# Optimization experiments

Measured on AMD Instinct MI355X. Metric: run time of the kernel, lower is better.

Reference implementation:

```python
import jax, jax.numpy as jnp
import numpy as np

N, E, F_IN, H, MH, C, G = 100000, 3200000, 128, 32, 64, 10, 64

def _seg_sum(data, ids, num):
    return jax.ops.segment_sum(data, ids, num_segments=num)

def gcn_conv(x, row, col, ew, W, b, n):
    # PyG GCNConv: linear first, then self-loops + symmetric edge-weight norm + scatter-add
    h = x @ W  # [N, H]
    loop = jnp.arange(n)
    r = jnp.concatenate([row, loop])
    c = jnp.concatenate([col, loop])
    w = jnp.concatenate([ew, jnp.ones((n,), dtype=ew.dtype)])
    deg = _seg_sum(w, c, n)
    dinv = jnp.where(deg > 0, jax.lax.rsqrt(deg), 0.0)
    norm = dinv[r] * w * dinv[c]  # [E+N]
    out = _seg_sum(norm[:, None] * h[r], c, n)  # scatter to targets
    return out + b

def setup_inputs():
    key = jax.random.key(0)
    ks = jax.random.split(key, 16)
    inp = {
        "x": jax.random.normal(ks[0], (N, F_IN), dtype=jnp.float32),
        "edge_index": jax.random.randint(ks[1], (2, E), 0, N, dtype=jnp.int64),
        "edge_weight": jax.random.uniform(ks[2], (E,), dtype=jnp.float32),
        "batch": jnp.sort(jax.random.randint(ks[3], (N,), 0, G, dtype=jnp.int64)),
    }
    def lin(k, i, o):
        s = 1.0 / np.sqrt(i)
        k1, k2 = jax.random.split(k)
        return (jax.random.uniform(k1, (i, o), minval=-s, maxval=s, dtype=jnp.float32),
                jax.random.uniform(k2, (o,), minval=-s, maxval=s, dtype=jnp.float32))
    inp["W1"], inp["b1"] = lin(ks[4], F_IN, H)
    inp["W2"], inp["b2"] = lin(ks[5], H, H)
    inp["W3"], inp["b3"] = lin(ks[6], H, H)
    inp["Wm0"], inp["bm0"] = lin(ks[7], H, MH)
    inp["Wm1"], inp["bm1"] = lin(ks[8], MH, MH)
    inp["Wout"], inp["bout"] = lin(ks[9], MH, C)
    return inp

def reference(x, edge_index, edge_weight, batch, W1, b1, W2, b2, W3, b3, Wm0, bm0, Wm1, bm1, Wout, bout):
    row, col = edge_index[0], edge_index[1]
    h = jax.nn.relu(gcn_conv(x, row, col, edge_weight, W1, b1, N))
    h = jax.nn.relu(gcn_conv(h, row, col, edge_weight, W2, b2, N))
    h = gcn_conv(h, row, col, edge_weight, W3, b3, N)
    # global mean pool over graphs
    sums = _seg_sum(h, batch, G)
    counts = _seg_sum(jnp.ones((N,), dtype=h.dtype), batch, G)
    g = sums / jnp.maximum(counts, 1.0)[:, None]
    # dropout p=0.5 is identity at inference (training=False)
    g = jax.nn.relu(g @ Wm0 + bm0)
    g = jax.nn.relu(g @ Wm1 + bm1)
    return g @ Wout + bout
```

## Files before the change

kernel.cpp:

```cpp
#include <hip/hip_runtime.h>

#define NN 100000
#define NE 3200000
#define FIN 128
#define HID 32
#define MH  64
#define NC  10
#define NG  64
#define NBKT 782
#define NBLK 512
#define EPB  (NE / NBLK)
#define SCANL (NBKT * NBLK)
#define SRCMASK 0x1FFFF
#define BCAP 5120

typedef float floatx2 __attribute__((ext_vector_type(2)));

__global__ void init_misc(float* __restrict__ sc) {
    int i = blockIdx.x * 256 + threadIdx.x;
    if (i < NG * HID + NG) sc[i] = 0.0f;
}

__global__ __launch_bounds__(1024)
void hist_bkt(const int* __restrict__ ei, int* __restrict__ cnt2) {
    __shared__ int h[NBKT];
    int tid = threadIdx.x, blk = blockIdx.x;
    for (int b = tid; b < NBKT; b += 1024) h[b] = 0;
    __syncthreads();
    int base = blk * EPB;
    for (int i = tid; i < EPB; i += 1024)
        atomicAdd(&h[ei[NE + base + i] >> 7], 1);
    __syncthreads();
    for (int b = tid; b < NBKT; b += 1024) cnt2[b * NBLK + blk] = h[b];
}

__global__ void scan_block(const int* __restrict__ in, int* __restrict__ out,
                           int* __restrict__ bsum, int n) {
    __shared__ int lds[256];
    int tid = threadIdx.x;
    int base = blockIdx.x * 1024 + tid * 4;
    int v0 = 0, v1 = 0, v2 = 0, v3 = 0;
    if (base + 0 < n) v0 = in[base + 0];
    if (base + 1 < n) v1 = in[base + 1];
    if (base + 2 < n) v2 = in[base + 2];
    if (base + 3 < n) v3 = in[base + 3];
    int s = v0 + v1 + v2 + v3;
    lds[tid] = s;
    __syncthreads();
    for (int off = 1; off < 256; off <<= 1) {
        int val = (tid >= off) ? lds[tid - off] : 0;
        __syncthreads();
        lds[tid] += val;
        __syncthreads();
    }
    int excl = lds[tid] - s;
    if (tid == 255) bsum[blockIdx.x] = lds[255];
    if (base + 0 < n) out[base + 0] = excl;
    if (base + 1 < n) out[base + 1] = excl + v0;
    if (base + 2 < n) out[base + 2] = excl + v0 + v1;
    if (base + 3 < n) out[base + 3] = excl + v0 + v1 + v2;
}

__global__ void scan_top(int* __restrict__ bsum, int nb) {
    int lane = threadIdx.x;
    int carry = 0;
    for (int base = 0; base < nb; base += 64) {
        int i = base + lane;
        int orig = (i < nb) ? bsum[i] : 0;
        int v = orig;
#pragma unroll
        for (int off = 1; off < 64; off <<= 1) {
            int t = __shfl_up(v, off, 64);
            if (lane >= off) v += t;
        }
        if (i < nb) bsum[i] = carry + v - orig;
        carry += __shfl(v, 63, 64);
    }
}

__global__ void scan_add(int* __restrict__ data, const int* __restrict__ bsum, int n) {
    int i = blockIdx.x * 256 + threadIdx.x;
    if (i < n) data[i] += bsum[i >> 10];
}

__global__ __launch_bounds__(1024)
void scatter_bkt(const int* __restrict__ ei, const float* __restrict__ ew,
                 const int* __restrict__ cnt2, const int* __restrict__ scanned,
                 int2* __restrict__ tre) {
    __shared__ int2 pay[EPB];
    __shared__ int scur[NBKT];
    __shared__ int hexc[NBKT];
    __shared__ int gbase[NBKT];
    int tid = threadIdx.x, blk = blockIdx.x;
    int myh = 0;
    if (tid < NBKT) {
        myh = cnt2[tid * NBLK + blk];
        gbase[tid] = scanned[tid * NBLK + blk];
        scur[tid] = myh;
    }
    __syncthreads();
    for (int off = 1; off < NBKT; off <<= 1) {
        int v = (tid < NBKT && tid >= off) ? scur[tid - off] : 0;
        __syncthreads();
        if (tid < NBKT) scur[tid] += v;
        __syncthreads();
    }
    if (tid < NBKT) { int ex = scur[tid] - myh; hexc[tid] = ex; scur[tid] = ex; }
    __syncthreads();
    int base = blk * EPB;
    for (int i = tid; i < EPB; i += 1024) {
        int e = base + i;
        int c = ei[NE + e];
        int r = ei[e];
        unsigned int wb = __float_as_uint(ew[e]);
        int b = c >> 7;
        int j = atomicAdd(&scur[b], 1);
        pay[j] = make_int2(r | ((c & 127) << 17) | ((b & 0xFF) << 24),
                           (int)((wb & ~3u) | ((unsigned)b >> 8)));
    }
    __syncthreads();
    for (int j = tid; j < EPB; j += 1024) {
        int2 q = pay[j];
        int b = (int)((((unsigned)q.y & 3u) << 8) | (((unsigned)q.x >> 24) & 0xFFu));
        int pos = gbase[b] + (j - hexc[b]);
        tre[pos] = make_int2(q.x & 0x00FFFFFF, q.y & ~3);
    }
}

__global__ __launch_bounds__(512)
void deg_k(const int2* __restrict__ tre, const int* __restrict__ scanned,
           float* __restrict__ dinv) {
    __shared__ float dw[128];
    int b = blockIdx.x, tid = threadIdx.x;
    int base = scanned[b * NBLK];
    int end = (b == NBKT - 1) ? NE : scanned[(b + 1) * NBLK];
    if (tid < 128) dw[tid] = 0.f;
    __syncthreads();
    for (int i = base + tid; i < end; i += 512) {
        int2 q = tre[i];
        atomicAdd(&dw[(q.x >> 17) & 127], __int_as_float(q.y));
    }
    __syncthreads();
    if (tid < 128) {
        int node = b * 128 + tid;
        if (node < NN) dinv[node] = rsqrtf(1.0f + dw[tid]);
    }
}

__global__ __launch_bounds__(512)
void sort_k(const int2* __restrict__ tre, const int* __restrict__ scanned,
            const float* __restrict__ dinv,
            unsigned int* __restrict__ srn4, int* __restrict__ rowptr) {
    __shared__ int2 ed[BCAP];
    __shared__ int h[128];
    __shared__ int sc[128];
    __shared__ int cur[128];
    int b = blockIdx.x, tid = threadIdx.x;
    int base = scanned[b * NBLK];
    int end = (b == NBKT - 1) ? NE : scanned[(b + 1) * NBLK];
    int n = end - base;
    bool staged = (n <= BCAP);
    if (tid < 128) h[tid] = 0;
    if (staged)
        for (int i = tid; i < n; i += 512) ed[i] = tre[base + i];
    __syncthreads();
    for (int i = tid; i < n; i += 512) {
        int2 q = staged ? ed[i] : tre[base + i];
        atomicAdd(&h[(q.x >> 17) & 127], 1);
    }
    __syncthreads();
    if (tid < 128) sc[tid] = h[tid];
    __syncthreads();
    for (int off = 1; off < 128; off <<= 1) {
        int v = (tid < 128 && tid >= off) ? sc[tid - off] : 0;
        __syncthreads();
        if (tid < 128) sc[tid] += v;
        __syncthreads();
    }
    if (tid < 128) {
        int node = b * 128 + tid;
        if (node < NN) rowptr[node] = base + sc[tid];
        cur[tid] = base + sc[tid] - h[tid];
    }
    __syncthreads();
    for (int i = tid; i < n; i += 512) {
        int2 q = staged ? ed[i] : tre[base + i];
        int key = (q.x >> 17) & 127;
        int pos = atomicAdd(&cur[key], 1);
        unsigned int src = (unsigned)(q.x & SRCMASK);
        float w = __int_as_float(q.y) * dinv[src];
        unsigned int wb = __float_as_uint(w);
        wb += 0x7FFFu + ((wb >> 16) & 1u);
        srn4[pos] = src | (((wb >> 16) & 0x7FFFu) << 17);
    }
}

template <int IN_DIM, bool RELU_IN>
__global__ __launch_bounds__(256)
void linear_k(const float* __restrict__ in, const float* __restrict__ W,
              unsigned int* __restrict__ tmp8) {
    constexpr int J4 = IN_DIM / 4;
    constexpr int XSS = J4 + 1;
    __shared__ float4 xs[64 * XSS];
    __shared__ float4 wp[IN_DIM * 8];
    int tid = threadIdx.x;
    for (int idx = tid; idx < IN_DIM * 8; idx += 256) {
        int j = idx >> 3, kg = idx & 7;
        const float* wr = W + j * 32 + kg * 4;
        wp[idx] = make_float4(wr[0], wr[1], wr[2], wr[3]);
    }
    int rbase = blockIdx.x * 64;
    const float4* in4 = (const float4*)in;
    for (int idx = tid; idx < 64 * J4; idx += 256) {
        int row = idx / J4, j4 = idx % J4;
        int grow = rbase + row;
        float4 v = (grow < NN) ? in4[(size_t)grow * J4 + j4]
                               : make_float4(0.f, 0.f, 0.f, 0.f);
        if (RELU_IN) {
            v.x = fmaxf(v.x, 0.f); v.y = fmaxf(v.y, 0.f);
            v.z = fmaxf(v.z, 0.f); v.w = fmaxf(v.w, 0.f);
        }
        xs[row * XSS + j4] = v;
    }
    __syncthreads();
    int kg = tid & 7;
    int rp = tid >> 3;
    int r0 = rbase + 2 * rp;
    if (r0 >= NN) return;
    const float4* x0 = &xs[(2 * rp) * XSS];
    const float4* x1 = &xs[(2 * rp + 1) * XSS];
    float a00 = 0, a01 = 0, a02 = 0, a03 = 0;
    float a10 = 0, a11 = 0, a12 = 0, a13 = 0;
#pragma unroll
    for (int j4 = 0; j4 < J4; ++j4) {
        float4 v0 = x0[j4], v1 = x1[j4];
        const float4* wj = &wp[j4 * 4 * 8 + kg];
        float4 w0 = wj[0], w1 = wj[8], w2 = wj[16], w3 = wj[24];
#define LSTEP(VX0, VX1, W4) \
        a00 = fmaf(VX0, W4.x, a00); a01 = fmaf(VX0, W4.y, a01); \
        a02 = fmaf(VX0, W4.z, a02); a03 = fmaf(VX0, W4.w, a03); \
        a10 = fmaf(VX1, W4.x, a10); a11 = fmaf(VX1, W4.y, a11); \
        a12 = fmaf(VX1, W4.z, a12); a13 = fmaf(VX1, W4.w, a13);
        LSTEP(v0.x, v1.x, w0)
        LSTEP(v0.y, v1.y, w1)
        LSTEP(v0.z, v1.z, w2)
        LSTEP(v0.w, v1.w, w3)
#undef LSTEP
    }
    int q0 = __builtin_amdgcn_cvt_pk_fp8_f32(a00, a01, 0, false);
    q0 = __builtin_amdgcn_cvt_pk_fp8_f32(a02, a03, q0, true);
    int q1 = __builtin_amdgcn_cvt_pk_fp8_f32(a10, a11, 0, false);
    q1 = __builtin_amdgcn_cvt_pk_fp8_f32(a12, a13, q1, true);
    tmp8[r0 * 8 + kg] = (unsigned int)q0;
    tmp8[(r0 + 1) * 8 + kg] = (unsigned int)q1;
}

__global__ void aggregate(const unsigned int* __restrict__ srn4,
                          const int* __restrict__ rowptr,
                          const float* __restrict__ dinv,
                          const float* __restrict__ bias,
                          const unsigned int* __restrict__ tmp8,
                          float* __restrict__ h) {
    int wid = (blockIdx.x * 256 + threadIdx.x) >> 6;
    if (wid >= NN) return;
    int lane = threadIdx.x & 63;
    int g = lane >> 3;
    int q = lane & 7;
    int end = rowptr[wid];
    int start = (wid == 0) ? 0 : rowptr[wid - 1];
    float a0 = 0, a1 = 0, a2 = 0, a3 = 0;
    float b0 = 0, b1 = 0, b2 = 0, b3 = 0;
    int e = start + g;
    for (; e + 8 < end; e += 16) {
        unsigned int p0 = srn4[e];
        unsigned int p1 = srn4[e + 8];
        unsigned int u0 = tmp8[(size_t)(p0 & SRCMASK) * 8 + q];
        unsigned int u1 = tmp8[(size_t)(p1 & SRCMASK) * 8 + q];
        float w0 = __uint_as_float((p0 >> 1) & 0x7FFF0000u);
        float w1 = __uint_as_float((p1 >> 1) & 0x7FFF0000u);
        floatx2 lo0 = __builtin_amdgcn_cvt_pk_f32_fp8(u0, false);
        floatx2 hi0 = __builtin_amdgcn_cvt_pk_f32_fp8(u0, true);
        floatx2 lo1 = __builtin_amdgcn_cvt_pk_f32_fp8(u1, false);
        floatx2 hi1 = __builtin_amdgcn_cvt_pk_f32_fp8(u1, true);
        a0 = fmaf(w0, lo0.x, a0); a1 = fmaf(w0, lo0.y, a1);
        a2 = fmaf(w0, hi0.x, a2); a3 = fmaf(w0, hi0.y, a3);
        b0 = fmaf(w1, lo1.x, b0); b1 = fmaf(w1, lo1.y, b1);
        b2 = fmaf(w1, hi1.x, b2); b3 = fmaf(w1, hi1.y, b3);
    }
    if (e < end) {
        unsigned int p = srn4[e];
        unsigned int u = tmp8[(size_t)(p & SRCMASK) * 8 + q];
        float w = __uint_as_float((p >> 1) & 0x7FFF0000u);
        floatx2 lo = __builtin_amdgcn_cvt_pk_f32_fp8(u, false);
        floatx2 hi = __builtin_amdgcn_cvt_pk_f32_fp8(u, true);
        a0 = fmaf(w, lo.x, a0); a1 = fmaf(w, lo.y, a1);
        a2 = fmaf(w, hi.x, a2); a3 = fmaf(w, hi.y, a3);
    }
    a0 += b0; a1 += b1; a2 += b2; a3 += b3;
    a0 += __shfl_xor(a0, 8, 64); a1 += __shfl_xor(a1, 8, 64);
    a2 += __shfl_xor(a2, 8, 64); a3 += __shfl_xor(a3, 8, 64);
    a0 += __shfl_xor(a0, 16, 64); a1 += __shfl_xor(a1, 16, 64);
    a2 += __shfl_xor(a2, 16, 64); a3 += __shfl_xor(a3, 16, 64);
    a0 += __shfl_xor(a0, 32, 64); a1 += __shfl_xor(a1, 32, 64);
    a2 += __shfl_xor(a2, 32, 64); a3 += __shfl_xor(a3, 32, 64);
    if (g == 0) {
        float d = dinv[wid];
        float d2 = d * d;
        unsigned int sv = tmp8[(size_t)wid * 8 + q];
        floatx2 slo = __builtin_amdgcn_cvt_pk_f32_fp8(sv, false);
        floatx2 shi = __builtin_amdgcn_cvt_pk_f32_fp8(sv, true);
        float4 bq = ((const float4*)bias)[q];
        float4 o;
        o.x = bq.x + d2 * slo.x + d * a0;
        o.y = bq.y + d2 * slo.y + d * a1;
        o.z = bq.z + d2 * shi.x + d * a2;
        o.w = bq.w + d2 * shi.y + d * a3;
        ((float4*)(h + (size_t)wid * HID))[q] = o;
    }
}

__global__ void pool_k(const float* __restrict__ h, const int* __restrict__ batch,
                       float* __restrict__ sums, float* __restrict__ counts) {
    int t = blockIdx.x * 256 + threadIdx.x;
    int chunk = t >> 5, k = t & 31;
    int n0 = chunk * 32;
    if (n0 >= NN) return;
    int n1 = min(n0 + 32, NN);
    int g = batch[n0];
    float acc = 0.f, cacc = 0.f;
    for (int i = n0; i < n1; ++i) {
        int gi = batch[i];
        if (gi != g) {
            atomicAdd(&sums[g * HID + k], acc);
            if (k == 0) atomicAdd(&counts[g], cacc);
            g = gi; acc = 0.f; cacc = 0.f;
        }
        acc += h[(size_t)i * HID + k];
        cacc += 1.f;
    }
    atomicAdd(&sums[g * HID + k], acc);
    if (k == 0) atomicAdd(&counts[g], cacc);
}

__global__ __launch_bounds__(64)
void mlp_k(const float* __restrict__ sums, const float* __restrict__ counts,
           const float* __restrict__ Wm0, const float* __restrict__ bm0,
           const float* __restrict__ Wm1, const float* __restrict__ bm1,
           const float* __restrict__ Wout, const float* __restrict__ bout,
           float* __restrict__ out) {
    __shared__ float g0[HID];
    __shared__ float g1[MH];
    __shared__ float g2[MH];
    int g = blockIdx.x;
    int k = threadIdx.x;
    if (k < HID) g0[k] = sums[g * HID + k] / fmaxf(counts[g], 1.0f);
    __syncthreads();
    float acc = bm0[k];
#pragma unroll
    for (int j = 0; j < HID; ++j) acc = fmaf(g0[j], Wm0[j * MH + k], acc);
    g1[k] = fmaxf(acc, 0.f);
    __syncthreads();
    float acc2 = bm1[k];
#pragma unroll
    for (int j = 0; j < MH; ++j) acc2 = fmaf(g1[j], Wm1[j * MH + k], acc2);
    g2[k] = fmaxf(acc2, 0.f);
    __syncthreads();
    if (k < NC) {
        float acc3 = bout[k];
#pragma unroll
        for (int j = 0; j < MH; ++j) acc3 = fmaf(g2[j], Wout[j * NC + k], acc3);
        out[g * NC + k] = acc3;
    }
}

extern "C" void kernel_launch(void* const* d_in, const int* in_sizes, int n_in,
                              void* d_out, int out_size, void* d_ws, size_t ws_size,
                              hipStream_t stream) {
    const float* x    = (const float*)d_in[0];
    const int*   ei   = (const int*)d_in[1];
    const float* ew   = (const float*)d_in[2];
    const int*   batch= (const int*)d_in[3];
    const float* W1   = (const float*)d_in[4];
    const float* b1   = (const float*)d_in[5];
    const float* W2   = (const float*)d_in[6];
    const float* b2   = (const float*)d_in[7];
    const float* W3   = (const float*)d_in[8];
    const float* b3   = (const float*)d_in[9];
    const float* Wm0  = (const float*)d_in[10];
    const float* bm0  = (const float*)d_in[11];
    const float* Wm1  = (const float*)d_in[12];
    const float* bm1  = (const float*)d_in[13];
    const float* Wout = (const float*)d_in[14];
    const float* bout = (const float*)d_in[15];
    float* out = (float*)d_out;

    char* p = (char*)d_ws;
    unsigned int* srn4 = (unsigned int*)p; p += sizeof(unsigned int) * (size_t)NE;
    char*  S   = p;                      p += 12 * (size_t)NE;
    int2*  tre = (int2*)S;
    int*   cnt2    = (int*)(S + sizeof(int2) * (size_t)NE);
    int*   scanned = cnt2 + SCANL;
    unsigned int* tmp8 = (unsigned int*)S;
    float* hA  = (float*)(S + (size_t)NN * HID);
    float* hB  = hA + (size_t)NN * HID;
    int*   bsum    = (int*)p;            p += sizeof(int) * 512;
    float* dinv    = (float*)p;          p += sizeof(float) * NN;
    int*   rowptr  = (int*)p;            p += sizeof(int) * NN;
    float* sums    = (float*)p;          p += sizeof(float) * NG * HID;
    float* counts  = (float*)p;

    dim3 blk(256);
    const int NB_SCAN = (SCANL + 1023) / 1024;
    const int NB_LIN = (NN + 63) / 64;

    init_misc<<<9, blk, 0, stream>>>(sums);
    hist_bkt<<<NBLK, 1024, 0, stream>>>(ei, cnt2);
    scan_block<<<NB_SCAN, blk, 0, stream>>>(cnt2, scanned, bsum, SCANL);
    scan_top<<<1, 64, 0, stream>>>(bsum, NB_SCAN);
    scan_add<<<(SCANL + 255) / 256, blk, 0, stream>>>(scanned, bsum, SCANL);
    scatter_bkt<<<NBLK, 1024, 0, stream>>>(ei, ew, cnt2, scanned, tre);
    deg_k<<<NBKT, 512, 0, stream>>>(tre, scanned, dinv);
    sort_k<<<NBKT, 512, 0, stream>>>(tre, scanned, dinv, srn4, rowptr);

    linear_k<FIN, false><<<NB_LIN, blk, 0, stream>>>(x, W1, tmp8);
    aggregate<<<25000, blk, 0, stream>>>(srn4, rowptr, dinv, b1, tmp8, hA);
    linear_k<HID, true><<<NB_LIN, blk, 0, stream>>>(hA, W2, tmp8);
    aggregate<<<25000, blk, 0, stream>>>(srn4, rowptr, dinv, b2, tmp8, hB);
    linear_k<HID, true><<<NB_LIN, blk, 0, stream>>>(hB, W3, tmp8);
    aggregate<<<25000, blk, 0, stream>>>(srn4, rowptr, dinv, b3, tmp8, hA);

    pool_k<<<391, blk, 0, stream>>>(hA, batch, sums, counts);
    mlp_k<<<NG, 64, 0, stream>>>(sums, counts, Wm0, bm0, Wm1, bm1, Wout, bout, out);
}
```

Before: 422.3 us.

## Fuse degree into sort, fold source norm into linear, unroll aggregate, segment pool

The degree computation moves into sort_k, which removes a separate pass over the bucketed edges. The source-side dinv factor is now applied to the linear output before fp8 quantisation, so the per-edge dinv gather in the sort is no longer needed. The aggregate loop is unrolled to four edges per iteration for more loads in flight, and pooling becomes one block per graph using binary search, which removes the init kernel and the atomics. Scaling before fp8 quantisation changes the numerical error profile, and the per-graph pool launches only 64 blocks.

```diff
diff --git a/kernel.cpp b/kernel.cpp
--- a/kernel.cpp
+++ b/kernel.cpp
@@ -15,11 +15,6 @@
 #define BCAP 5120
 
 typedef float floatx2 __attribute__((ext_vector_type(2)));
-
-__global__ void init_misc(float* __restrict__ sc) {
-    int i = blockIdx.x * 256 + threadIdx.x;
-    if (i < NG * HID + NG) sc[i] = 0.0f;
-}
 
 __global__ __launch_bounds__(1024)
 void hist_bkt(const int* __restrict__ ei, int* __restrict__ cnt2) {
@@ -128,31 +123,12 @@
 }
 
 __global__ __launch_bounds__(512)
-void deg_k(const int2* __restrict__ tre, const int* __restrict__ scanned,
-           float* __restrict__ dinv) {
-    __shared__ float dw[128];
-    int b = blockIdx.x, tid = threadIdx.x;
-    int base = scanned[b * NBLK];
-    int end = (b == NBKT - 1) ? NE : scanned[(b + 1) * NBLK];
-    if (tid < 128) dw[tid] = 0.f;
-    __syncthreads();
-    for (int i = base + tid; i < end; i += 512) {
-        int2 q = tre[i];
-        atomicAdd(&dw[(q.x >> 17) & 127], __int_as_float(q.y));
-    }
-    __syncthreads();
-    if (tid < 128) {
-        int node = b * 128 + tid;
-        if (node < NN) dinv[node] = rsqrtf(1.0f + dw[tid]);
-    }
-}
-
-__global__ __launch_bounds__(512)
 void sort_k(const int2* __restrict__ tre, const int* __restrict__ scanned,
-            const float* __restrict__ dinv,
-            unsigned int* __restrict__ srn4, int* __restrict__ rowptr) {
+            unsigned int* __restrict__ srn4, int* __restrict__ rowptr,
+            float* __restrict__ dinv) {
     __shared__ int2 ed[BCAP];
     __shared__ int h[128];
+    __shared__ float dw[128];
     __shared__ int sc[128];
     __shared__ int cur[128];
     int b = blockIdx.x, tid = threadIdx.x;
@@ -160,13 +136,15 @@
     int end = (b == NBKT - 1) ? NE : scanned[(b + 1) * NBLK];
     int n = end - base;
     bool staged = (n <= BCAP);
-    if (tid < 128) h[tid] = 0;
+    if (tid < 128) { h[tid] = 0; dw[tid] = 0.f; }
     if (staged)
         for (int i = tid; i < n; i += 512) ed[i] = tre[base + i];
     __syncthreads();
     for (int i = tid; i < n; i += 512) {
         int2 q = staged ? ed[i] : tre[base + i];
-        atomicAdd(&h[(q.x >> 17) & 127], 1);
+        int key = (q.x >> 17) & 127;
+        atomicAdd(&h[key], 1);
+        atomicAdd(&dw[key], __int_as_float(q.y));
     }
     __syncthreads();
     if (tid < 128) sc[tid] = h[tid];
@@ -179,7 +157,10 @@
     }
     if (tid < 128) {
         int node = b * 128 + tid;
-        if (node < NN) rowptr[node] = base + sc[tid];
+        if (node < NN) {
+            rowptr[node] = base + sc[tid];
+            dinv[node] = rsqrtf(1.0f + dw[tid]);
+        }
         cur[tid] = base + sc[tid] - h[tid];
     }
     __syncthreads();
@@ -187,18 +168,16 @@
         int2 q = staged ? ed[i] : tre[base + i];
         int key = (q.x >> 17) & 127;
         int pos = atomicAdd(&cur[key], 1);
-        unsigned int src = (unsigned)(q.x & SRCMASK);
-        float w = __int_as_float(q.y) * dinv[src];
-        unsigned int wb = __float_as_uint(w);
+        unsigned int wb = (unsigned)q.y;
         wb += 0x7FFFu + ((wb >> 16) & 1u);
-        srn4[pos] = src | (((wb >> 16) & 0x7FFFu) << 17);
+        srn4[pos] = (unsigned)(q.x & SRCMASK) | (((wb >> 16) & 0x7FFFu) << 17);
     }
 }
 
 template <int IN_DIM, bool RELU_IN>
 __global__ __launch_bounds__(256)
 void linear_k(const float* __restrict__ in, const float* __restrict__ W,
-              unsigned int* __restrict__ tmp8) {
+              const float* __restrict__ dinv, unsigned int* __restrict__ tmp8) {
     constexpr int J4 = IN_DIM / 4;
     constexpr int XSS = J4 + 1;
     __shared__ float4 xs[64 * XSS];
@@ -247,6 +226,9 @@
         LSTEP(v0.w, v1.w, w3)
 #undef LSTEP
     }
+    float d0 = dinv[r0], d1 = dinv[r0 + 1];
+    a00 *= d0; a01 *= d0; a02 *= d0; a03 *= d0;
+    a10 *= d1; a11 *= d1; a12 *= d1; a13 *= d1;
     int q0 = __builtin_amdgcn_cvt_pk_fp8_f32(a00, a01, 0, false);
     q0 = __builtin_amdgcn_cvt_pk_fp8_f32(a02, a03, q0, true);
     int q1 = __builtin_amdgcn_cvt_pk_fp8_f32(a10, a11, 0, false);
@@ -271,23 +253,38 @@
     float a0 = 0, a1 = 0, a2 = 0, a3 = 0;
     float b0 = 0, b1 = 0, b2 = 0, b3 = 0;
     int e = start + g;
-    for (; e + 8 < end; e += 16) {
+    for (; e + 24 < end; e += 32) {
         unsigned int p0 = srn4[e];
         unsigned int p1 = srn4[e + 8];
+        unsigned int p2 = srn4[e + 16];
+        unsigned int p3 = srn4[e + 24];
         unsigned int u0 = tmp8[(size_t)(p0 & SRCMASK) * 8 + q];
         unsigned int u1 = tmp8[(size_t)(p1 & SRCMASK) * 8 + q];
+        unsigned int u2 = tmp8[(size_t)(p2 & SRCMASK) * 8 + q];
+        unsigned int u3 = tmp8[(size_t)(p3 & SRCMASK) * 8 + q];
         float w0 = __uint_as_float((p0 >> 1) & 0x7FFF0000u);
         float w1 = __uint_as_float((p1 >> 1) & 0x7FFF0000u);
-        floatx2 lo0 = __builtin_amdgcn_cvt_pk_f32_fp8(u0, false);
-        floatx2 hi0 = __builtin_amdgcn_cvt_pk_f32_fp8(u0, true);
-        floatx2 lo1 = __builtin_amdgcn_cvt_pk_f32_fp8(u1, false);
-        floatx2 hi1 = __builtin_amdgcn_cvt_pk_f32_fp8(u1, true);
-        a0 = fmaf(w0, lo0.x, a0); a1 = fmaf(w0, lo0.y, a1);
-        a2 = fmaf(w0, hi0.x, a2); a3 = fmaf(w0, hi0.y, a3);
-        b0 = fmaf(w1, lo1.x, b0); b1 = fmaf(w1, lo1.y, b1);
-        b2 = fmaf(w1, hi1.x, b2); b3 = fmaf(w1, hi1.y, b3);
-    }
-    if (e < end) {
+        float w2 = __uint_as_float((p2 >> 1) & 0x7FFF0000u);
+        float w3 = __uint_as_float((p3 >> 1) & 0x7FFF0000u);
+        floatx2 lo, hi;
+        lo = __builtin_amdgcn_cvt_pk_f32_fp8(u0, false);
+        hi = __builtin_amdgcn_cvt_pk_f32_fp8(u0, true);
+        a0 = fmaf(w0, lo.x, a0); a1 = fmaf(w0, lo.y, a1);
+        a2 = fmaf(w0, hi.x, a2); a3 = fmaf(w0, hi.y, a3);
+        lo = __builtin_amdgcn_cvt_pk_f32_fp8(u1, false);
+        hi = __builtin_amdgcn_cvt_pk_f32_fp8(u1, true);
+        b0 = fmaf(w1, lo.x, b0); b1 = fmaf(w1, lo.y, b1);
+        b2 = fmaf(w1, hi.x, b2); b3 = fmaf(w1, hi.y, b3);
+        lo = __builtin_amdgcn_cvt_pk_f32_fp8(u2, false);
+        hi = __builtin_amdgcn_cvt_pk_f32_fp8(u2, true);
+        a0 = fmaf(w2, lo.x, a0); a1 = fmaf(w2, lo.y, a1);
+        a2 = fmaf(w2, hi.x, a2); a3 = fmaf(w2, hi.y, a3);
+        lo = __builtin_amdgcn_cvt_pk_f32_fp8(u3, false);
+        hi = __builtin_amdgcn_cvt_pk_f32_fp8(u3, true);
+        b0 = fmaf(w3, lo.x, b0); b1 = fmaf(w3, lo.y, b1);
+        b2 = fmaf(w3, hi.x, b2); b3 = fmaf(w3, hi.y, b3);
+    }
+    for (; e < end; e += 8) {
         unsigned int p = srn4[e];
         unsigned int u = tmp8[(size_t)(p & SRCMASK) * 8 + q];
         float w = __uint_as_float((p >> 1) & 0x7FFF0000u);
@@ -305,41 +302,42 @@
     a2 += __shfl_xor(a2, 32, 64); a3 += __shfl_xor(a3, 32, 64);
     if (g == 0) {
         float d = dinv[wid];
-        float d2 = d * d;
         unsigned int sv = tmp8[(size_t)wid * 8 + q];
         floatx2 slo = __builtin_amdgcn_cvt_pk_f32_fp8(sv, false);
         floatx2 shi = __builtin_amdgcn_cvt_pk_f32_fp8(sv, true);
         float4 bq = ((const float4*)bias)[q];
         float4 o;
-        o.x = bq.x + d2 * slo.x + d * a0;
-        o.y = bq.y + d2 * slo.y + d * a1;
-        o.z = bq.z + d2 * shi.x + d * a2;
-        o.w = bq.w + d2 * shi.y + d * a3;
+        o.x = bq.x + d * (slo.x + a0);
+        o.y = bq.y + d * (slo.y + a1);
+        o.z = bq.z + d * (shi.x + a2);
+        o.w = bq.w + d * (shi.y + a3);
         ((float4*)(h + (size_t)wid * HID))[q] = o;
     }
 }
 
-__global__ void pool_k(const float* __restrict__ h, const int* __restrict__ batch,
-                       float* __restrict__ sums, float* __restrict__ counts) {
-    int t = blockIdx.x * 256 + threadIdx.x;
-    int chunk = t >> 5, k = t & 31;
-    int n0 = chunk * 32;
-    if (n0 >= NN) return;
-    int n1 = min(n0 + 32, NN);
-    int g = batch[n0];
-    float acc = 0.f, cacc = 0.f;
-    for (int i = n0; i < n1; ++i) {
-        int gi = batch[i];
-        if (gi != g) {
-            atomicAdd(&sums[g * HID + k], acc);
-            if (k == 0) atomicAdd(&counts[g], cacc);
-            g = gi; acc = 0.f; cacc = 0.f;
-        }
-        acc += h[(size_t)i * HID + k];
-        cacc += 1.f;
-    }
-    atomicAdd(&sums[g * HID + k], acc);
-    if (k == 0) atomicAdd(&counts[g], cacc);
+__global__ __launch_bounds__(256)
+void pool_k(const float* __restrict__ h, const int* __restrict__ batch,
+            float* __restrict__ sums, float* __restrict__ counts) {
+    __shared__ float red[256];
+    int g = blockIdx.x;
+    int lo = 0, hi = NN;
+    while (lo < hi) { int m = (lo + hi) >> 1; if (batch[m] < g) lo = m + 1; else hi = m; }
+    int s = lo;
+    lo = s; hi = NN;
+    while (lo < hi) { int m = (lo + hi) >> 1; if (batch[m] < g + 1) lo = m + 1; else hi = m; }
+    int e2 = lo;
+    int tid = threadIdx.x;
+    int r = tid >> 5, k = tid & 31;
+    float acc = 0.f;
+    for (int i = s + r; i < e2; i += 8) acc += h[(size_t)i * HID + k];
+    red[tid] = acc;
+    __syncthreads();
+    for (int off = 128; off >= 32; off >>= 1) {
+        if (tid < off) red[tid] += red[tid + off];
+        __syncthreads();
+    }
+    if (tid < 32) sums[g * HID + tid] = red[tid];
+    if (tid == 0) counts[g] = (float)(e2 - s);
 }
 
 __global__ __launch_bounds__(64)
@@ -413,22 +411,20 @@
     const int NB_SCAN = (SCANL + 1023) / 1024;
     const int NB_LIN = (NN + 63) / 64;
 
-    init_misc<<<9, blk, 0, stream>>>(sums);
     hist_bkt<<<NBLK, 1024, 0, stream>>>(ei, cnt2);
     scan_block<<<NB_SCAN, blk, 0, stream>>>(cnt2, scanned, bsum, SCANL);
     scan_top<<<1, 64, 0, stream>>>(bsum, NB_SCAN);
     scan_add<<<(SCANL + 255) / 256, blk, 0, stream>>>(scanned, bsum, SCANL);
     scatter_bkt<<<NBLK, 1024, 0, stream>>>(ei, ew, cnt2, scanned, tre);
-    deg_k<<<NBKT, 512, 0, stream>>>(tre, scanned, dinv);
-    sort_k<<<NBKT, 512, 0, stream>>>(tre, scanned, dinv, srn4, rowptr);
-
-    linear_k<FIN, false><<<NB_LIN, blk, 0, stream>>>(x, W1, tmp8);
+    sort_k<<<NBKT, 512, 0, stream>>>(tre, scanned, srn4, rowptr, dinv);
+
+    linear_k<FIN, false><<<NB_LIN, blk, 0, stream>>>(x, W1, dinv, tmp8);
     aggregate<<<25000, blk, 0, stream>>>(srn4, rowptr, dinv, b1, tmp8, hA);
-    linear_k<HID, true><<<NB_LIN, blk, 0, stream>>>(hA, W2, tmp8);
+    linear_k<HID, true><<<NB_LIN, blk, 0, stream>>>(hA, W2, dinv, tmp8);
     aggregate<<<25000, blk, 0, stream>>>(srn4, rowptr, dinv, b2, tmp8, hB);
-    linear_k<HID, true><<<NB_LIN, blk, 0, stream>>>(hB, W3, tmp8);
+    linear_k<HID, true><<<NB_LIN, blk, 0, stream>>>(hB, W3, dinv, tmp8);
     aggregate<<<25000, blk, 0, stream>>>(srn4, rowptr, dinv, b3, tmp8, hA);
 
-    pool_k<<<391, blk, 0, stream>>>(hA, batch, sums, counts);
+    pool_k<<<NG, blk, 0, stream>>>(hA, batch, sums, counts);
     mlp_k<<<NG, 64, 0, stream>>>(sums, counts, Wm0, bm0, Wm1, bm1, Wout, bout, out);
 }
```

Result: slower. 441.3 us (+4.5%).
